# Optimization experiments

Hardware: AMD Instinct MI355X
Metric: run time of the kernel (lower is better)

## Reference

```python
import jax, jax.numpy as jnp
import numpy as np

D_EQUI = 64
D_INV = 256
D_MSG = 64
N_HEADS = 32
D_HEAD = D_INV // N_HEADS
D_FF = 256
D_EDGE_IN = 64
D_EDGE_OUT = 64
D_OUT = D_EQUI + N_HEADS + D_EDGE_OUT  # 160
IN_FEATS = 2 * D_MSG + D_EQUI + D_EDGE_IN  # 256
B, N = 4, 256


def setup_inputs() -> dict:
    key = jax.random.key(0)
    ks = jax.random.split(key, 20)
    s = 0.05
    inp = {
        "equis": jax.random.normal(ks[0], (B, N, 3, D_EQUI), jnp.float32),
        "invs": jax.random.normal(ks[1], (B, N, D_INV), jnp.float32),
        "edges": jax.random.normal(ks[2], (B, N, N, D_EDGE_IN), jnp.float32),
        "adj_matrix": jnp.ones((B, N, N), jnp.int32),
        # _PairwiseMessages params
        "qW": jax.random.normal(ks[3], (D_INV, D_MSG), jnp.float32) * s,
        "qb": jnp.zeros((D_MSG,), jnp.float32),
        "kW": jax.random.normal(ks[4], (D_INV, D_MSG), jnp.float32) * s,
        "kb": jnp.zeros((D_MSG,), jnp.float32),
        "mW1": jax.random.normal(ks[5], (IN_FEATS, D_FF), jnp.float32) * s,
        "mb1": jnp.zeros((D_FF,), jnp.float32),
        "mW2": jax.random.normal(ks[6], (D_FF, D_OUT), jnp.float32) * s,
        "mb2": jnp.zeros((D_OUT,), jnp.float32),
        # _InvAttention params
        "inv_inW": jax.random.normal(ks[7], (D_INV, D_INV), jnp.float32) * s,
        "inv_inb": jnp.zeros((D_INV,), jnp.float32),
        "inv_outW": jax.random.normal(ks[8], (D_INV, D_INV), jnp.float32) * s,
        "inv_outb": jnp.zeros((D_INV,), jnp.float32),
        # _EquiAttention params (no bias)
        "equi_inW": jax.random.normal(ks[9], (D_EQUI, D_EQUI), jnp.float32) * s,
        "equi_outW": jax.random.normal(ks[10], (D_EQUI, D_EQUI), jnp.float32) * s,
    }
    return inp


def _forward(equis, invs, edges, adj_matrix, qW, qb, kW, kb, mW1, mb1, mW2, mb2,
             inv_inW, inv_inb, inv_outW, inv_outb, equi_inW, equi_outW):
    # ---- pairwise messages ----
    # dotprods of equivariant 3-vectors per channel: [B, Nq, Nk, d_equi]
    dot = jnp.einsum("bqdc,bkdc->bqkc", equis, equis)
    qm = invs @ qW + qb  # [B,N,d_msg]
    km = invs @ kW + kb
    Nn = invs.shape[1]
    feats = jnp.concatenate([
        jnp.broadcast_to(qm[:, :, None, :], (qm.shape[0], Nn, Nn, D_MSG)),
        jnp.broadcast_to(km[:, None, :, :], (km.shape[0], Nn, Nn, D_MSG)),
        dot,
        edges,
    ], axis=-1)  # [B,N,N,in_feats]
    msgs = jax.nn.silu(feats @ mW1 + mb1) @ mW2 + mb2  # [B,N,N,d_out]

    # adjacency -> additive mask (0 where connected, -inf otherwise)
    mask = jnp.where(adj_matrix == 0, -jnp.inf, 0.0).astype(msgs.dtype)

    # ---- invariant attention (first n_heads channels) ----
    inv_msgs = msgs[..., :N_HEADS] + mask[..., None]
    attn_i = jax.nn.softmax(inv_msgs, axis=2)  # softmax over kv
    hf = (invs @ inv_inW + inv_inb).reshape(invs.shape[0], Nn, N_HEADS, D_HEAD)
    out_i = jnp.einsum("bqkh,bkhd->bqhd", attn_i, hf)
    w_i = jnp.sqrt(jnp.sum(attn_i * attn_i, axis=2))  # [B,q,H]
    out_i = out_i * w_i[..., None]
    inv_updates = out_i.reshape(invs.shape[0], Nn, D_INV) @ inv_outW + inv_outb

    # ---- equivariant attention (next d_equi channels) ----
    equi_msgs = msgs[..., N_HEADS:N_HEADS + D_EQUI] + mask[..., None]
    attn_e = jax.nn.softmax(equi_msgs, axis=2)  # [B,q,k,c]
    pe = equis @ equi_inW  # [B,N,3,d_equi]
    out_e = jnp.einsum("bqkc,bkdc->bqdc", attn_e, pe)
    w_e = jnp.sqrt(jnp.sum(attn_e * attn_e, axis=2))  # [B,q,c]
    out_e = out_e * w_e[:, :, None, :]
    equi_updates = out_e @ equi_outW  # [B,N,3,d_equi]

    # ---- edge updates (remaining channels) ----
    edge_updates = msgs[..., N_HEADS + D_EQUI:]
    return equi_updates, inv_updates, edge_updates


def reference(equis, invs, edges, adj_matrix, qW, qb, kW, kb, mW1, mb1, mW2, mb2,
              inv_inW, inv_inb, inv_outW, inv_outb, equi_inW, equi_outW):
    return _forward(equis, invs, edges, adj_matrix, qW, qb, kW, kb, mW1, mb1, mW2, mb2,
                    inv_inW, inv_inb, inv_outW, inv_outb, equi_inW, equi_outW)
```

## Files before the change

kernel.cpp:

```cpp
#include <hip/hip_runtime.h>
#include <hip/hip_bf16.h>
#include <math.h>


typedef __attribute__((ext_vector_type(8))) short short8;
typedef __attribute__((ext_vector_type(8))) __bf16 bf16x8;
typedef __attribute__((ext_vector_type(4))) float f32x4;

constexpr int EQUI_OFF = 0;
constexpr int INV_OFF  = 196608;
constexpr int EDGE_OFF = 458752;

__device__ __forceinline__ unsigned short f2bf(float x) {
    unsigned u = __builtin_bit_cast(unsigned, x);
    u = u + 0x7FFFu + ((u >> 16) & 1u);
    return (unsigned short)(u >> 16);
}
__device__ __forceinline__ float bf2f(unsigned short u) {
    return __builtin_bit_cast(float, ((unsigned)u) << 16);
}
__device__ __forceinline__ unsigned short f2bfh(float x) {
    return __builtin_bit_cast(unsigned short, (__bf16)x);
}
__device__ __forceinline__ unsigned pk2(float a, float b) {
    return (unsigned)f2bfh(a) | ((unsigned)f2bfh(b) << 16);
}
__device__ __forceinline__ short8 pk8(f32x4 a, f32x4 b) {
    bf16x8 r = { (__bf16)a.x, (__bf16)a.y, (__bf16)a.z, (__bf16)a.w,
                 (__bf16)b.x, (__bf16)b.y, (__bf16)b.z, (__bf16)b.w };
    return __builtin_bit_cast(short8, r);
}
__device__ __forceinline__ f32x4 MFMA(short8 a, short8 b, f32x4 c) {
    return __builtin_amdgcn_mfma_f32_16x16x32_bf16(
        __builtin_bit_cast(bf16x8, a), __builtin_bit_cast(bf16x8, b), c, 0, 0, 0);
}

__global__ void prep_weights(const float* __restrict__ mW1, const float* __restrict__ mW2,
                             short* __restrict__ W1T, short* __restrict__ W2T) {
    int idx = blockIdx.x * 256 + threadIdx.x;
    if (idx < 32768) {
        int n = idx >> 7, kk = idx & 127;
        W1T[idx] = (short)f2bf(mW1[(128 + kk) * 256 + n]);
    } else {
        int i2 = idx - 32768;
        int n = i2 >> 8, f = i2 & 255;
        W2T[i2] = (short)f2bf(mW2[f * 160 + n]);
    }
}

__global__ void prep_proj(const float* __restrict__ invs, const float* __restrict__ equis,
                          const float* __restrict__ qW, const float* __restrict__ qb,
                          const float* __restrict__ kW, const float* __restrict__ kb,
                          const float* __restrict__ inv_inW, const float* __restrict__ inv_inb,
                          const float* __restrict__ equi_inW,
                          float* __restrict__ qm, float* __restrict__ km,
                          float* __restrict__ hf, float* __restrict__ pe) {
    int tid = threadIdx.x;
    if (blockIdx.x < 1024) {
        int r = blockIdx.x;
        __shared__ float sInv[256];
        sInv[tid] = invs[r * 256 + tid];
        __syncthreads();
        if (tid < 64) {
            float acc = qb[tid];
            for (int f = 0; f < 256; ++f) acc += sInv[f] * qW[f * 64 + tid];
            qm[r * 64 + tid] = acc;
        } else if (tid < 128) {
            int c = tid - 64;
            float acc = kb[c];
            for (int f = 0; f < 256; ++f) acc += sInv[f] * kW[f * 64 + c];
            km[r * 64 + c] = acc;
        }
        float acch = inv_inb[tid];
        for (int f = 0; f < 256; ++f) acch += sInv[f] * inv_inW[f * 256 + tid];
        hf[r * 256 + tid] = acch;
    } else {
        int rn = blockIdx.x - 1024;
        if (tid < 192) {
            int d = tid >> 6, c = tid & 63;
            const float* erow = equis + (size_t)rn * 192 + d * 64;
            float acc = 0.f;
            for (int f = 0; f < 64; ++f) acc += erow[f] * equi_inW[f * 64 + c];
            pe[rn * 192 + d * 64 + c] = acc;
        }
    }
}

__global__ void prep_c12(const float* __restrict__ qm, const float* __restrict__ km,
                         const float* __restrict__ mW1, const float* __restrict__ mb1,
                         float* __restrict__ c1, float* __restrict__ c2) {
    int tid = threadIdx.x;
    __shared__ float s[64];
    if (blockIdx.x < 1024) {
        int r = blockIdx.x;
        if (tid < 64) s[tid] = qm[r * 64 + tid];
        __syncthreads();
        float acc = mb1[tid];
        #pragma unroll 8
        for (int k = 0; k < 64; ++k) acc = fmaf(s[k], mW1[k * 256 + tid], acc);
        c1[r * 256 + tid] = acc;
    } else {
        int r = blockIdx.x - 1024;
        if (tid < 64) s[tid] = km[r * 64 + tid];
        __syncthreads();
        float acc = 0.f;
        #pragma unroll 8
        for (int k = 0; k < 64; ++k) acc = fmaf(s[k], mW1[(64 + k) * 256 + tid], acc);
        c2[r * 256 + tid] = acc;
    }
}

__global__ void prep_T(const float* __restrict__ hf, const float* __restrict__ pe,
                       const float* __restrict__ inv_outW, const float* __restrict__ equi_outW,
                       unsigned short* __restrict__ hfT, unsigned short* __restrict__ peT,
                       unsigned short* __restrict__ WoT, unsigned short* __restrict__ EoT) {
    __shared__ float sT[64][65];
    int tid = threadIdx.x, bi = blockIdx.x;
    if (bi < 64) {
        int b = bi >> 4, t = bi & 15, tj = t >> 2, th = t & 3;
        #pragma unroll
        for (int i = 0; i < 16; ++i) { int idx = i * 256 + tid; int jl = idx >> 6, hl = idx & 63;
            sT[jl][hl] = hf[((size_t)(b * 256 + tj * 64 + jl)) * 256 + th * 64 + hl]; }
        __syncthreads();
        #pragma unroll
        for (int i = 0; i < 16; ++i) { int idx = i * 256 + tid; int hl = idx >> 6, jl = idx & 63;
            hfT[((size_t)(b * 256 + th * 64 + hl)) * 256 + tj * 64 + jl] = f2bf(sT[jl][hl]); }
    } else if (bi < 128) {
        int i2 = bi - 64; int b = i2 >> 4, t = i2 & 15, tj = t >> 2, d = t & 3;
        if (d == 3) {
            #pragma unroll
            for (int i = 0; i < 16; ++i) { int idx = i * 256 + tid; int c = idx >> 6, jl = idx & 63;
                peT[((size_t)((b * 64 + c) * 4 + 3)) * 256 + tj * 64 + jl] = 0; }
        } else {
            #pragma unroll
            for (int i = 0; i < 16; ++i) { int idx = i * 256 + tid; int jl = idx >> 6, c = idx & 63;
                sT[jl][c] = pe[((size_t)(b * 256 + tj * 64 + jl)) * 192 + d * 64 + c]; }
            __syncthreads();
            #pragma unroll
            for (int i = 0; i < 16; ++i) { int idx = i * 256 + tid; int c = idx >> 6, jl = idx & 63;
                peT[((size_t)((b * 64 + c) * 4 + d)) * 256 + tj * 64 + jl] = f2bf(sT[jl][c]); }
        }
    } else if (bi < 144) {
        int i2 = bi - 128; int tf = i2 >> 2, tn = i2 & 3;
        #pragma unroll
        for (int i = 0; i < 16; ++i) { int idx = i * 256 + tid; int fl = idx >> 6, nl = idx & 63;
            sT[fl][nl] = inv_outW[(size_t)(tf * 64 + fl) * 256 + tn * 64 + nl]; }
        __syncthreads();
        #pragma unroll
        for (int i = 0; i < 16; ++i) { int idx = i * 256 + tid; int nl = idx >> 6, fl = idx & 63;
            WoT[(size_t)(tn * 64 + nl) * 256 + tf * 64 + fl] = f2bf(sT[fl][nl]); }
    } else {
        #pragma unroll
        for (int i = 0; i < 16; ++i) { int idx = i * 256 + tid; int cl = idx >> 6, c2 = idx & 63;
            sT[cl][c2] = equi_outW[cl * 64 + c2]; }
        __syncthreads();
        #pragma unroll
        for (int i = 0; i < 16; ++i) { int idx = i * 256 + tid; int c2 = idx >> 6, cl = idx & 63;
            EoT[c2 * 64 + cl] = f2bf(sT[cl][c2]); }
    }
}

constexpr int GA_AH   = 0;
constexpr int GA_EQ   = 32768;
constexpr int GA_MASK = 33536;
constexpr int GA_BYTES = 33792;

__launch_bounds__(256, 4)
__global__ void semla_gemm(const float* __restrict__ equis, const float* __restrict__ edges,
                           const int* __restrict__ adj, const float* __restrict__ mb2,
                           const short* __restrict__ W1T, const short* __restrict__ W2T,
                           const float* __restrict__ c1, const float* __restrict__ c2,
                           float* __restrict__ out, unsigned short* __restrict__ PT) {
    extern __shared__ char smem[];
    float* sEQ   = (float*)(smem + GA_EQ);
    float* sMask = (float*)(smem + GA_MASK);

    const int tid  = threadIdx.x;
    const int lane = tid & 63;
    const int w    = tid >> 6;
    const int bid  = blockIdx.x;
    const int bq   = bid >> 2;
    const int jc   = bid & 3;
    const int b    = bq >> 8;

    const int lrow = lane & 15;
    const int kgrp = (lane >> 4) << 3;
    const int drow = (lane >> 4) << 2;

    if (tid < 192) sEQ[tid] = equis[(size_t)bq * 192 + tid];
    if (tid < 64)  sMask[tid] = adj[(size_t)bq * 256 + (jc << 6) + tid] ? 0.f : -1e30f;

    float c1v[4];
    #pragma unroll
    for (int ni = 0; ni < 4; ++ni)
        c1v[ni] = c1[bq * 256 + (w << 6) + (ni << 4) + lrow];
    const int ntiles = (w < 2) ? 3 : 2;
    const int nbase  = (w < 2) ? w * 48 : 96 + (w - 2) * 32;
    float b2v[3];
    #pragma unroll
    for (int ti = 0; ti < 3; ++ti)
        if (ti < ntiles) b2v[ti] = mb2[nbase + (ti << 4) + lrow];

    auto stA16 = [&](int row, int colbyte, short8 v) {
        int byte = ((row << 8) + colbyte) ^ ((row & 7) << 4);
        *(short8*)(smem + GA_AH + byte) = v;
    };
    auto ldA = [&](int row, int kb) -> short8 {
        int byte = ((row << 8) + (kb << 1)) ^ ((row & 7) << 4);
        return *(const short8*)(smem + GA_AH + byte);
    };
    auto stH = [&](int row, int col, unsigned short v) {
        int byte = ((row << 9) + (col << 1)) ^ ((row & 7) << 4);
        *(unsigned short*)(smem + GA_AH + byte) = v;
    };
    auto ldH = [&](int row, int kb) -> short8 {
        int byte = ((row << 9) + (kb << 1)) ^ ((row & 7) << 4);
        return *(const short8*)(smem + GA_AH + byte);
    };

    __syncthreads();

    {
        int r = tid >> 2, h = tid & 3;
        const float* erow = equis + (size_t)((b << 8) + (jc << 6) + r) * 192;
        #pragma unroll
        for (int g = 0; g < 2; ++g) {
            int cg = h + g * 4;
            f32x4 lo = (f32x4)(0.f), hi = (f32x4)(0.f);
            #pragma unroll
            for (int d = 0; d < 3; ++d) {
                f32x4 e0 = *(const f32x4*)(erow + d * 64 + cg * 8);
                f32x4 e1 = *(const f32x4*)(erow + d * 64 + cg * 8 + 4);
                f32x4 q0 = *(const f32x4*)(sEQ + d * 64 + cg * 8);
                f32x4 q1 = *(const f32x4*)(sEQ + d * 64 + cg * 8 + 4);
                lo += e0 * q0; hi += e1 * q1;
            }
            stA16(r, cg * 16, pk8(lo, hi));
        }
        const float* ebase = edges + ((size_t)bq * 256 + (jc << 6)) * 64;
        #pragma unroll
        for (int g = 0; g < 2; ++g) {
            int c8 = h + g * 4;
            f32x4 e0 = *(const f32x4*)(ebase + r * 64 + c8 * 8);
            f32x4 e1 = *(const f32x4*)(ebase + r * 64 + c8 * 8 + 4);
            stA16(r, 128 + c8 * 16, pk8(e0, e1));
        }
    }
    __syncthreads();

    f32x4 acc[4][4];
    #pragma unroll
    for (int mi = 0; mi < 4; ++mi)
        #pragma unroll
        for (int ni = 0; ni < 4; ++ni) acc[mi][ni] = (f32x4)(0.f);

    #pragma unroll
    for (int k0 = 0; k0 < 128; k0 += 32) {
        int kb = k0 + kgrp;
        short8 a0 = ldA(lrow, kb), a1 = ldA(16 + lrow, kb),
               a2 = ldA(32 + lrow, kb), a3 = ldA(48 + lrow, kb);
        short8 bf[4];
        #pragma unroll
        for (int ni = 0; ni < 4; ++ni)
            bf[ni] = *(const short8*)(W1T + ((w << 6) + (ni << 4) + lrow) * 128 + kb);
        #pragma unroll
        for (int ni = 0; ni < 4; ++ni) {
            acc[0][ni] = MFMA(a0, bf[ni], acc[0][ni]);
            acc[1][ni] = MFMA(a1, bf[ni], acc[1][ni]);
            acc[2][ni] = MFMA(a2, bf[ni], acc[2][ni]);
            acc[3][ni] = MFMA(a3, bf[ni], acc[3][ni]);
        }
    }
    __syncthreads();

    const float* c2base = c2 + ((size_t)((b << 8) + (jc << 6)) << 8);
    #pragma unroll
    for (int mi = 0; mi < 4; ++mi)
        #pragma unroll
        for (int r = 0; r < 4; ++r) {
            int row = (mi << 4) + drow + r;
            const float* c2row = c2base + (row << 8);
            #pragma unroll
            for (int ni = 0; ni < 4; ++ni) {
                int n = (w << 6) + (ni << 4) + lrow;
                float x = acc[mi][ni][r] + c1v[ni] + c2row[n];
                float hh = x * __builtin_amdgcn_rcpf(1.f + __expf(-x));
                stH(row, n, f2bfh(hh));
            }
        }
    __syncthreads();

    f32x4 acc2[4][3];
    #pragma unroll
    for (int mi = 0; mi < 4; ++mi)
        #pragma unroll
        for (int ti = 0; ti < 3; ++ti) acc2[mi][ti] = (f32x4)(0.f);

    #pragma unroll
    for (int k0 = 0; k0 < 256; k0 += 32) {
        int kb = k0 + kgrp;
        short8 a0 = ldH(lrow, kb), a1 = ldH(16 + lrow, kb),
               a2 = ldH(32 + lrow, kb), a3 = ldH(48 + lrow, kb);
        short8 bt[3];
        #pragma unroll
        for (int ti = 0; ti < 3; ++ti)
            if (ti < ntiles) bt[ti] = *(const short8*)(W2T + (nbase + (ti << 4) + lrow) * 256 + kb);
        #pragma unroll
        for (int ti = 0; ti < 3; ++ti)
            if (ti < ntiles) {
                acc2[0][ti] = MFMA(a0, bt[ti], acc2[0][ti]);
                acc2[1][ti] = MFMA(a1, bt[ti], acc2[1][ti]);
                acc2[2][ti] = MFMA(a2, bt[ti], acc2[2][ti]);
                acc2[3][ti] = MFMA(a3, bt[ti], acc2[3][ti]);
            }
    }
    __syncthreads();

    if (w < 2) {
        #pragma unroll
        for (int ti = 0; ti < 3; ++ti) {
            int n = nbase + (ti << 4) + lrow;
            float bias = b2v[ti];
            #pragma unroll
            for (int mi = 0; mi < 4; ++mi) {
                int j0 = (mi << 4) + drow;
                f32x4 mv = *(const f32x4*)(sMask + j0);
                unsigned lo = pk2(acc2[mi][ti][0] + bias + mv.x,
                                  acc2[mi][ti][1] + bias + mv.y);
                unsigned hi = pk2(acc2[mi][ti][2] + bias + mv.z,
                                  acc2[mi][ti][3] + bias + mv.w);
                *(unsigned*)(smem + n * 136 + j0 * 2)     = lo;
                *(unsigned*)(smem + n * 136 + j0 * 2 + 4) = hi;
            }
        }
    } else {
        #pragma unroll
        for (int mi = 0; mi < 4; ++mi)
            #pragma unroll
            for (int ti = 0; ti < 2; ++ti) {
                int n = nbase + (ti << 4) + lrow;
                #pragma unroll
                for (int r = 0; r < 4; ++r) {
                    int j = (jc << 6) + (mi << 4) + drow + r;
                    out[EDGE_OFF + ((size_t)bq * 256 + j) * 64 + (n - 96)] = acc2[mi][ti][r] + b2v[ti];
                }
            }
    }
    __syncthreads();

    if (tid < 192) {
        int n = tid >> 1, half = tid & 1;
        const char* src = smem + n * 136 + half * 64;
        unsigned short* dst = PT + (((size_t)bq * 96 + n) << 8) + (jc << 6) + half * 32;
        #pragma unroll
        for (int i = 0; i < 4; ++i)
            *(short8*)(dst + i * 8) = *(const short8*)(src + i * 16);
    }
}

constexpr int ES_A = 0;
constexpr int ES_W = 32768;
constexpr int ES_BYTES = 33024;

__launch_bounds__(256, 4)
__global__ void semla_einsum(const unsigned short* __restrict__ PT,
                             const unsigned short* __restrict__ hfT,
                             const unsigned short* __restrict__ peT,
                             unsigned short* __restrict__ OIb, unsigned short* __restrict__ OEb) {
    extern __shared__ char smem[];
    float* sW = (float*)(smem + ES_W);
    const int tid = threadIdx.x, lane = tid & 63, w = tid >> 6;
    const int bi = blockIdx.x;
    const int qc = bi & 3;
    const int t  = bi >> 2;
    const int b  = t / 96;
    const int c  = t - 96 * b;
    const int lrow = lane & 15, kgrp = (lane >> 4) << 3, drow = (lane >> 4) << 2;

    #pragma unroll
    for (int i = 0; i < 8; ++i) {
        int id = i * 256 + tid; int row = id >> 5, ck = id & 31;
        size_t src = (((size_t)((b << 8) + (qc << 6) + row) * 96 + c) << 8) + ck * 16;
        short8 v = *(const short8*)(PT + src);
        int byte = ((row << 9) + (ck << 4)) ^ ((row & 7) << 4);
        *(short8*)(smem + ES_A + byte) = v;
    }
    __syncthreads();

    {
        int r = tid >> 2, p = tid & 3;
        float v[64];
        #pragma unroll
        for (int i = 0; i < 8; ++i) {
            int ck = p * 8 + i;
            int byte = ((r << 9) + (ck << 4)) ^ ((r & 7) << 4);
            short8 x = *(const short8*)(smem + ES_A + byte);
            #pragma unroll
            for (int e = 0; e < 8; ++e) v[i * 8 + e] = bf2f((unsigned short)x[e]);
        }
        float m = v[0];
        #pragma unroll
        for (int i = 1; i < 64; ++i) m = fmaxf(m, v[i]);
        m = fmaxf(m, __shfl_xor(m, 1)); m = fmaxf(m, __shfl_xor(m, 2));
        float s = 0.f, q = 0.f;
        #pragma unroll
        for (int i = 0; i < 64; ++i) { float e = __expf(v[i] - m); v[i] = e; s += e; q = fmaf(e, e, q); }
        s += __shfl_xor(s, 1); s += __shfl_xor(s, 2);
        q += __shfl_xor(q, 1); q += __shfl_xor(q, 2);
        float rs = (s > 0.f) ? 1.f / s : 0.f;
        if (p == 0) sW[r] = sqrtf(q) * rs;
        #pragma unroll
        for (int i = 0; i < 8; ++i) {
            int ck = p * 8 + i;
            short8 o;
            #pragma unroll
            for (int e = 0; e < 8; ++e) o[e] = (short)f2bfh(v[i * 8 + e] * rs);
            int byte = ((r << 9) + (ck << 4)) ^ ((r & 7) << 4);
            *(short8*)(smem + ES_A + byte) = o;
        }
    }
    __syncthreads();

    const unsigned short* Bbase =
        (c < 32) ? hfT + (((size_t)((b << 8) + (c << 3) + (lrow & 7))) << 8)
                 : peT + (((size_t)((((b << 6) + (c - 32)) << 2) + (lrow & 3))) << 8);
    f32x4 acc = (f32x4)(0.f);
    #pragma unroll
    for (int k0 = 0; k0 < 256; k0 += 32) {
        int kb = k0 + kgrp;
        int byte = ((((w << 4) + lrow) << 9) + (kb << 1)) ^ ((lrow & 7) << 4);
        short8 a = *(const short8*)(smem + ES_A + byte);
        short8 bb = *(const short8*)(Bbase + kb);
        acc = MFMA(a, bb, acc);
    }
    const int nvalid = (c < 32) ? 8 : 3;
    if (lrow < nvalid) {
        #pragma unroll
        for (int r2 = 0; r2 < 4; ++r2) {
            int ql = (w << 4) + drow + r2;
            float val = acc[r2] * sW[ql];
            size_t grow = (size_t)((b << 8) + (qc << 6) + ql);
            if (c < 32) OIb[(grow << 8) + (c << 3) + lrow] = f2bfh(val);
            else        OEb[(grow * 3 + lrow) * 64 + (c - 32)] = f2bfh(val);
        }
    }
}

constexpr int PJ_BYTES = 32768;

__launch_bounds__(256, 4)
__global__ void semla_proj(const unsigned short* __restrict__ OIb,
                           const unsigned short* __restrict__ OEb,
                           const unsigned short* __restrict__ WoT,
                           const unsigned short* __restrict__ EoT,
                           const float* __restrict__ inv_outb, float* __restrict__ out) {
    extern __shared__ char smem[];
    const int tid = threadIdx.x, lane = tid & 63, w = tid >> 6;
    const int lrow = lane & 15, kgrp = (lane >> 4) << 3, drow = (lane >> 4) << 2;
    const int bi = blockIdx.x;

    if (bi < 32) {
        const int mb = bi >> 1, nb = bi & 1;
        #pragma unroll
        for (int i = 0; i < 8; ++i) {
            int id = i * 256 + tid; int row = id >> 5, ck = id & 31;
            short8 v = *(const short8*)(OIb + (((size_t)(mb * 64 + row)) << 8) + ck * 16);
            int byte = ((row << 9) + (ck << 4)) ^ ((row & 7) << 4);
            *(short8*)(smem + byte) = v;
        }
        __syncthreads();
        f32x4 acc[4][2];
        #pragma unroll
        for (int mi = 0; mi < 4; ++mi)
            #pragma unroll
            for (int ti = 0; ti < 2; ++ti) acc[mi][ti] = (f32x4)(0.f);
        #pragma unroll
        for (int k0 = 0; k0 < 256; k0 += 32) {
            int kb = k0 + kgrp;
            short8 a[4];
            #pragma unroll
            for (int mi = 0; mi < 4; ++mi) {
                int byte = ((((mi << 4) + lrow) << 9) + (kb << 1)) ^ ((lrow & 7) << 4);
                a[mi] = *(const short8*)(smem + byte);
            }
            #pragma unroll
            for (int ti = 0; ti < 2; ++ti) {
                int n = nb * 128 + w * 32 + (ti << 4) + lrow;
                short8 bb = *(const short8*)(WoT + n * 256 + kb);
                #pragma unroll
                for (int mi = 0; mi < 4; ++mi) acc[mi][ti] = MFMA(a[mi], bb, acc[mi][ti]);
            }
        }
        #pragma unroll
        for (int ti = 0; ti < 2; ++ti) {
            int n = nb * 128 + w * 32 + (ti << 4) + lrow;
            float bias = inv_outb[n];
            #pragma unroll
            for (int mi = 0; mi < 4; ++mi)
                #pragma unroll
                for (int r = 0; r < 4; ++r) {
                    int row = mb * 64 + (mi << 4) + drow + r;
                    out[INV_OFF + (size_t)row * 256 + n] = acc[mi][ti][r] + bias;
                }
        }
    } else {
        const int mb = bi - 32;
        #pragma unroll
        for (int i = 0; i < 2; ++i) {
            int id = i * 256 + tid; int row = id >> 3, ck = id & 7;
            short8 v = *(const short8*)(OEb + (((size_t)(mb * 64 + row)) << 6) + ck * 16);
            int byte = ((row << 7) + (ck << 4)) ^ ((row & 7) << 4);
            *(short8*)(smem + byte) = v;
        }
        __syncthreads();
        f32x4 acc[4];
        #pragma unroll
        for (int ni = 0; ni < 4; ++ni) acc[ni] = (f32x4)(0.f);
        #pragma unroll
        for (int k0 = 0; k0 < 64; k0 += 32) {
            int kb = k0 + kgrp;
            int byte = ((((w << 4) + lrow) << 7) + (kb << 1)) ^ ((lrow & 7) << 4);
            short8 a = *(const short8*)(smem + byte);
            #pragma unroll
            for (int ni = 0; ni < 4; ++ni) {
                short8 bb = *(const short8*)(EoT + ((ni << 4) + lrow) * 64 + kb);
                acc[ni] = MFMA(a, bb, acc[ni]);
            }
        }
        #pragma unroll
        for (int ni = 0; ni < 4; ++ni)
            #pragma unroll
            for (int r = 0; r < 4; ++r) {
                int rowg = mb * 64 + (w << 4) + drow + r;
                int bq = rowg / 3, d = rowg - 3 * bq;
                out[EQUI_OFF + (size_t)bq * 192 + d * 64 + (ni << 4) + lrow] = acc[ni][r];
            }
    }
}

extern "C" void kernel_launch(void* const* d_in, const int* in_sizes, int n_in,
                              void* d_out, int out_size, void* d_ws, size_t ws_size,
                              hipStream_t stream) {
    const float* equis    = (const float*)d_in[0];
    const float* invs     = (const float*)d_in[1];
    const float* edges    = (const float*)d_in[2];
    const int*   adj      = (const int*)d_in[3];
    const float* qW       = (const float*)d_in[4];
    const float* qb       = (const float*)d_in[5];
    const float* kW       = (const float*)d_in[6];
    const float* kb       = (const float*)d_in[7];
    const float* mW1      = (const float*)d_in[8];
    const float* mb1      = (const float*)d_in[9];
    const float* mW2      = (const float*)d_in[10];
    const float* mb2      = (const float*)d_in[11];
    const float* inv_inW  = (const float*)d_in[12];
    const float* inv_inb  = (const float*)d_in[13];
    const float* inv_outW = (const float*)d_in[14];
    const float* inv_outb = (const float*)d_in[15];
    const float* equi_inW = (const float*)d_in[16];
    const float* equi_outW= (const float*)d_in[17];

    char* ws = (char*)d_ws;
    short* W1T = (short*)(ws + 0);
    short* W2T = (short*)(ws + 65536);
    float* qm  = (float*)(ws + 147456);
    float* km  = (float*)(ws + 409600);
    float* hf  = (float*)(ws + 671744);
    float* pe  = (float*)(ws + 1720320);
    float* c1  = (float*)(ws + 2506752);
    float* c2  = (float*)(ws + 3555328);
    unsigned short* PT  = (unsigned short*)(ws + 4603904);
    unsigned short* peT = (unsigned short*)(ws + 54935552);
    unsigned short* hfT = (unsigned short*)(ws + 147456);
    unsigned short* OIb = (unsigned short*)(ws + 55459840);
    unsigned short* OEb = (unsigned short*)(ws + 55984128);
    unsigned short* WoT = (unsigned short*)(ws + 56377344);
    unsigned short* EoT = (unsigned short*)(ws + 56508416);

    prep_weights<<<288, 256, 0, stream>>>(mW1, mW2, W1T, W2T);
    prep_proj<<<2048, 256, 0, stream>>>(invs, equis, qW, qb, kW, kb,
                                        inv_inW, inv_inb, equi_inW, qm, km, hf, pe);
    prep_c12<<<2048, 256, 0, stream>>>(qm, km, mW1, mb1, c1, c2);
    prep_T<<<145, 256, 0, stream>>>(hf, pe, inv_outW, equi_outW, hfT, peT, WoT, EoT);
    semla_gemm<<<4096, 256, GA_BYTES, stream>>>(equis, edges, adj, mb2, W1T, W2T,
                                                c1, c2, (float*)d_out, PT);
    semla_einsum<<<1536, 256, ES_BYTES, stream>>>(PT, hfT, peT, OIb, OEb);
    semla_proj<<<80, 256, PJ_BYTES, stream>>>(OIb, OEb, WoT, EoT, inv_outb, (float*)d_out);
}
```

Before: 167.2 us.

## Merge prep kernels and loop semla_gemm over key chunks with edge prefetch

```diff
diff --git a/kernel.cpp b/kernel.cpp
--- a/kernel.cpp
+++ b/kernel.cpp
@@ -35,29 +35,18 @@
         __builtin_bit_cast(bf16x8, a), __builtin_bit_cast(bf16x8, b), c, 0, 0, 0);
 }
 
-__global__ void prep_weights(const float* __restrict__ mW1, const float* __restrict__ mW2,
-                             short* __restrict__ W1T, short* __restrict__ W2T) {
-    int idx = blockIdx.x * 256 + threadIdx.x;
-    if (idx < 32768) {
-        int n = idx >> 7, kk = idx & 127;
-        W1T[idx] = (short)f2bf(mW1[(128 + kk) * 256 + n]);
-    } else {
-        int i2 = idx - 32768;
-        int n = i2 >> 8, f = i2 & 255;
-        W2T[i2] = (short)f2bf(mW2[f * 160 + n]);
-    }
-}
-
-__global__ void prep_proj(const float* __restrict__ invs, const float* __restrict__ equis,
-                          const float* __restrict__ qW, const float* __restrict__ qb,
-                          const float* __restrict__ kW, const float* __restrict__ kb,
-                          const float* __restrict__ inv_inW, const float* __restrict__ inv_inb,
-                          const float* __restrict__ equi_inW,
-                          float* __restrict__ qm, float* __restrict__ km,
-                          float* __restrict__ hf, float* __restrict__ pe) {
-    int tid = threadIdx.x;
-    if (blockIdx.x < 1024) {
-        int r = blockIdx.x;
+__global__ void prep1(const float* __restrict__ invs, const float* __restrict__ equis,
+                      const float* __restrict__ qW, const float* __restrict__ qb,
+                      const float* __restrict__ kW, const float* __restrict__ kb,
+                      const float* __restrict__ inv_inW, const float* __restrict__ inv_inb,
+                      const float* __restrict__ equi_inW,
+                      const float* __restrict__ mW1, const float* __restrict__ mW2,
+                      float* __restrict__ qm, float* __restrict__ km,
+                      float* __restrict__ hf, float* __restrict__ pe,
+                      short* __restrict__ W1T, short* __restrict__ W2T) {
+    int tid = threadIdx.x, bi = blockIdx.x;
+    if (bi < 1024) {
+        int r = bi;
         __shared__ float sInv[256];
         sInv[tid] = invs[r * 256 + tid];
         __syncthreads();
@@ -74,8 +63,8 @@
         float acch = inv_inb[tid];
         for (int f = 0; f < 256; ++f) acch += sInv[f] * inv_inW[f * 256 + tid];
         hf[r * 256 + tid] = acch;
-    } else {
-        int rn = blockIdx.x - 1024;
+    } else if (bi < 2048) {
+        int rn = bi - 1024;
         if (tid < 192) {
             int d = tid >> 6, c = tid & 63;
             const float* erow = equis + (size_t)rn * 192 + d * 64;
@@ -83,87 +72,95 @@
             for (int f = 0; f < 64; ++f) acc += erow[f] * equi_inW[f * 64 + c];
             pe[rn * 192 + d * 64 + c] = acc;
         }
-    }
-}
-
-__global__ void prep_c12(const float* __restrict__ qm, const float* __restrict__ km,
-                         const float* __restrict__ mW1, const float* __restrict__ mb1,
-                         float* __restrict__ c1, float* __restrict__ c2) {
-    int tid = threadIdx.x;
-    __shared__ float s[64];
-    if (blockIdx.x < 1024) {
-        int r = blockIdx.x;
-        if (tid < 64) s[tid] = qm[r * 64 + tid];
+    } else {
+        int idx = (bi - 2048) * 256 + tid;
+        if (idx < 32768) {
+            int n = idx >> 7, kk = idx & 127;
+            W1T[idx] = (short)f2bf(mW1[(128 + kk) * 256 + n]);
+        } else {
+            int i2 = idx - 32768;
+            int n = i2 >> 8, f = i2 & 255;
+            W2T[i2] = (short)f2bf(mW2[f * 160 + n]);
+        }
+    }
+}
+
+__global__ void prep2(const float* __restrict__ qm, const float* __restrict__ km,
+                      const float* __restrict__ mW1, const float* __restrict__ mb1,
+                      const float* __restrict__ hf, const float* __restrict__ pe,
+                      const float* __restrict__ inv_outW, const float* __restrict__ equi_outW,
+                      float* __restrict__ c1, float* __restrict__ c2,
+                      unsigned short* __restrict__ hfT, unsigned short* __restrict__ peT,
+                      unsigned short* __restrict__ WoT, unsigned short* __restrict__ EoT) {
+    __shared__ float sT[64][65];
+    int tid = threadIdx.x, bi = blockIdx.x;
+    if (bi < 1024) {
+        int r = bi;
+        if (tid < 64) sT[0][tid] = qm[r * 64 + tid];
         __syncthreads();
         float acc = mb1[tid];
         #pragma unroll 8
-        for (int k = 0; k < 64; ++k) acc = fmaf(s[k], mW1[k * 256 + tid], acc);
+        for (int k = 0; k < 64; ++k) acc = fmaf(sT[0][k], mW1[k * 256 + tid], acc);
         c1[r * 256 + tid] = acc;
-    } else {
-        int r = blockIdx.x - 1024;
-        if (tid < 64) s[tid] = km[r * 64 + tid];
+    } else if (bi < 2048) {
+        int r = bi - 1024;
+        if (tid < 64) sT[0][tid] = km[r * 64 + tid];
         __syncthreads();
         float acc = 0.f;
         #pragma unroll 8
-        for (int k = 0; k < 64; ++k) acc = fmaf(s[k], mW1[(64 + k) * 256 + tid], acc);
+        for (int k = 0; k < 64; ++k) acc = fmaf(sT[0][k], mW1[(64 + k) * 256 + tid], acc);
         c2[r * 256 + tid] = acc;
-    }
-}
-
-__global__ void prep_T(const float* __restrict__ hf, const float* __restrict__ pe,
-                       const float* __restrict__ inv_outW, const float* __restrict__ equi_outW,
-                       unsigned short* __restrict__ hfT, unsigned short* __restrict__ peT,
-                       unsigned short* __restrict__ WoT, unsigned short* __restrict__ EoT) {
-    __shared__ float sT[64][65];
-    int tid = threadIdx.x, bi = blockIdx.x;
-    if (bi < 64) {
-        int b = bi >> 4, t = bi & 15, tj = t >> 2, th = t & 3;
-        #pragma unroll
-        for (int i = 0; i < 16; ++i) { int idx = i * 256 + tid; int jl = idx >> 6, hl = idx & 63;
-            sT[jl][hl] = hf[((size_t)(b * 256 + tj * 64 + jl)) * 256 + th * 64 + hl]; }
-        __syncthreads();
-        #pragma unroll
-        for (int i = 0; i < 16; ++i) { int idx = i * 256 + tid; int hl = idx >> 6, jl = idx & 63;
-            hfT[((size_t)(b * 256 + th * 64 + hl)) * 256 + tj * 64 + jl] = f2bf(sT[jl][hl]); }
-    } else if (bi < 128) {
-        int i2 = bi - 64; int b = i2 >> 4, t = i2 & 15, tj = t >> 2, d = t & 3;
-        if (d == 3) {
-            #pragma unroll
-            for (int i = 0; i < 16; ++i) { int idx = i * 256 + tid; int c = idx >> 6, jl = idx & 63;
-                peT[((size_t)((b * 64 + c) * 4 + 3)) * 256 + tj * 64 + jl] = 0; }
+    } else {
+        int bt = bi - 2048;
+        if (bt < 64) {
+            int b = bt >> 4, t = bt & 15, tj = t >> 2, th = t & 3;
+            #pragma unroll
+            for (int i = 0; i < 16; ++i) { int idx = i * 256 + tid; int jl = idx >> 6, hl = idx & 63;
+                sT[jl][hl] = hf[((size_t)(b * 256 + tj * 64 + jl)) * 256 + th * 64 + hl]; }
+            __syncthreads();
+            #pragma unroll
+            for (int i = 0; i < 16; ++i) { int idx = i * 256 + tid; int hl = idx >> 6, jl = idx & 63;
+                hfT[((size_t)(b * 256 + th * 64 + hl)) * 256 + tj * 64 + jl] = f2bf(sT[jl][hl]); }
+        } else if (bt < 128) {
+            int i2 = bt - 64; int b = i2 >> 4, t = i2 & 15, tj = t >> 2, d = t & 3;
+            if (d == 3) {
+                #pragma unroll
+                for (int i = 0; i < 16; ++i) { int idx = i * 256 + tid; int c = idx >> 6, jl = idx & 63;
+                    peT[((size_t)((b * 64 + c) * 4 + 3)) * 256 + tj * 64 + jl] = 0; }
+            } else {
+                #pragma unroll
+                for (int i = 0; i < 16; ++i) { int idx = i * 256 + tid; int jl = idx >> 6, c = idx & 63;
+                    sT[jl][c] = pe[((size_t)(b * 256 + tj * 64 + jl)) * 192 + d * 64 + c]; }
+                __syncthreads();
+                #pragma unroll
+                for (int i = 0; i < 16; ++i) { int idx = i * 256 + tid; int c = idx >> 6, jl = idx & 63;
+                    peT[((size_t)((b * 64 + c) * 4 + d)) * 256 + tj * 64 + jl] = f2bf(sT[jl][c]); }
+            }
+        } else if (bt < 144) {
+            int i2 = bt - 128; int tf = i2 >> 2, tn = i2 & 3;
+            #pragma unroll
+            for (int i = 0; i < 16; ++i) { int idx = i * 256 + tid; int fl = idx >> 6, nl = idx & 63;
+                sT[fl][nl] = inv_outW[(size_t)(tf * 64 + fl) * 256 + tn * 64 + nl]; }
+            __syncthreads();
+            #pragma unroll
+            for (int i = 0; i < 16; ++i) { int idx = i * 256 + tid; int nl = idx >> 6, fl = idx & 63;
+                WoT[(size_t)(tn * 64 + nl) * 256 + tf * 64 + fl] = f2bf(sT[fl][nl]); }
         } else {
             #pragma unroll
-            for (int i = 0; i < 16; ++i) { int idx = i * 256 + tid; int jl = idx >> 6, c = idx & 63;
-                sT[jl][c] = pe[((size_t)(b * 256 + tj * 64 + jl)) * 192 + d * 64 + c]; }
+            for (int i = 0; i < 16; ++i) { int idx = i * 256 + tid; int cl = idx >> 6, c2i = idx & 63;
+                sT[cl][c2i] = equi_outW[cl * 64 + c2i]; }
             __syncthreads();
             #pragma unroll
-            for (int i = 0; i < 16; ++i) { int idx = i * 256 + tid; int c = idx >> 6, jl = idx & 63;
-                peT[((size_t)((b * 64 + c) * 4 + d)) * 256 + tj * 64 + jl] = f2bf(sT[jl][c]); }
-        }
-    } else if (bi < 144) {
-        int i2 = bi - 128; int tf = i2 >> 2, tn = i2 & 3;
-        #pragma unroll
-        for (int i = 0; i < 16; ++i) { int idx = i * 256 + tid; int fl = idx >> 6, nl = idx & 63;
-            sT[fl][nl] = inv_outW[(size_t)(tf * 64 + fl) * 256 + tn * 64 + nl]; }
-        __syncthreads();
-        #pragma unroll
-        for (int i = 0; i < 16; ++i) { int idx = i * 256 + tid; int nl = idx >> 6, fl = idx & 63;
-            WoT[(size_t)(tn * 64 + nl) * 256 + tf * 64 + fl] = f2bf(sT[fl][nl]); }
-    } else {
-        #pragma unroll
-        for (int i = 0; i < 16; ++i) { int idx = i * 256 + tid; int cl = idx >> 6, c2 = idx & 63;
-            sT[cl][c2] = equi_outW[cl * 64 + c2]; }
-        __syncthreads();
-        #pragma unroll
-        for (int i = 0; i < 16; ++i) { int idx = i * 256 + tid; int c2 = idx >> 6, cl = idx & 63;
-            EoT[c2 * 64 + cl] = f2bf(sT[cl][c2]); }
+            for (int i = 0; i < 16; ++i) { int idx = i * 256 + tid; int c2i = idx >> 6, cl = idx & 63;
+                EoT[c2i * 64 + cl] = f2bf(sT[cl][c2i]); }
+        }
     }
 }
 
 constexpr int GA_AH   = 0;
 constexpr int GA_EQ   = 32768;
 constexpr int GA_MASK = 33536;
-constexpr int GA_BYTES = 33792;
+constexpr int GA_BYTES = 34560;
 
 __launch_bounds__(256, 4)
 __global__ void semla_gemm(const float* __restrict__ equis, const float* __restrict__ edges,
@@ -178,17 +175,26 @@
     const int tid  = threadIdx.x;
     const int lane = tid & 63;
     const int w    = tid >> 6;
-    const int bid  = blockIdx.x;
-    const int bq   = bid >> 2;
-    const int jc   = bid & 3;
+    const int bq   = (blockIdx.x & 7) * 128 + (blockIdx.x >> 3);
     const int b    = bq >> 8;
 
     const int lrow = lane & 15;
     const int kgrp = (lane >> 4) << 3;
     const int drow = (lane >> 4) << 2;
+    const int r    = tid >> 2, h = tid & 3;
+
+    const float* ebq = edges + (size_t)bq * 16384;
+    f32x4 ed0, ed1, ed2, ed3;
+    {
+        const float* eb = ebq + r * 64;
+        ed0 = *(const f32x4*)(eb + h * 8);
+        ed1 = *(const f32x4*)(eb + h * 8 + 4);
+        ed2 = *(const f32x4*)(eb + (h + 4) * 8);
+        ed3 = *(const f32x4*)(eb + (h + 4) * 8 + 4);
+    }
 
     if (tid < 192) sEQ[tid] = equis[(size_t)bq * 192 + tid];
-    if (tid < 64)  sMask[tid] = adj[(size_t)bq * 256 + (jc << 6) + tid] ? 0.f : -1e30f;
+    sMask[tid] = adj[(size_t)bq * 256 + tid] ? 0.f : -1e30f;
 
     float c1v[4];
     #pragma unroll
@@ -218,143 +224,148 @@
         return *(const short8*)(smem + GA_AH + byte);
     };
 
-    __syncthreads();
-
-    {
-        int r = tid >> 2, h = tid & 3;
-        const float* erow = equis + (size_t)((b << 8) + (jc << 6) + r) * 192;
-        #pragma unroll
-        for (int g = 0; g < 2; ++g) {
-            int cg = h + g * 4;
-            f32x4 lo = (f32x4)(0.f), hi = (f32x4)(0.f);
-            #pragma unroll
-            for (int d = 0; d < 3; ++d) {
-                f32x4 e0 = *(const f32x4*)(erow + d * 64 + cg * 8);
-                f32x4 e1 = *(const f32x4*)(erow + d * 64 + cg * 8 + 4);
-                f32x4 q0 = *(const f32x4*)(sEQ + d * 64 + cg * 8);
-                f32x4 q1 = *(const f32x4*)(sEQ + d * 64 + cg * 8 + 4);
-                lo += e0 * q0; hi += e1 * q1;
-            }
-            stA16(r, cg * 16, pk8(lo, hi));
-        }
-        const float* ebase = edges + ((size_t)bq * 256 + (jc << 6)) * 64;
-        #pragma unroll
-        for (int g = 0; g < 2; ++g) {
-            int c8 = h + g * 4;
-            f32x4 e0 = *(const f32x4*)(ebase + r * 64 + c8 * 8);
-            f32x4 e1 = *(const f32x4*)(ebase + r * 64 + c8 * 8 + 4);
-            stA16(r, 128 + c8 * 16, pk8(e0, e1));
-        }
-    }
-    __syncthreads();
-
-    f32x4 acc[4][4];
-    #pragma unroll
-    for (int mi = 0; mi < 4; ++mi)
-        #pragma unroll
-        for (int ni = 0; ni < 4; ++ni) acc[mi][ni] = (f32x4)(0.f);
-
-    #pragma unroll
-    for (int k0 = 0; k0 < 128; k0 += 32) {
-        int kb = k0 + kgrp;
-        short8 a0 = ldA(lrow, kb), a1 = ldA(16 + lrow, kb),
-               a2 = ldA(32 + lrow, kb), a3 = ldA(48 + lrow, kb);
-        short8 bf[4];
-        #pragma unroll
-        for (int ni = 0; ni < 4; ++ni)
-            bf[ni] = *(const short8*)(W1T + ((w << 6) + (ni << 4) + lrow) * 128 + kb);
-        #pragma unroll
-        for (int ni = 0; ni < 4; ++ni) {
-            acc[0][ni] = MFMA(a0, bf[ni], acc[0][ni]);
-            acc[1][ni] = MFMA(a1, bf[ni], acc[1][ni]);
-            acc[2][ni] = MFMA(a2, bf[ni], acc[2][ni]);
-            acc[3][ni] = MFMA(a3, bf[ni], acc[3][ni]);
-        }
-    }
-    __syncthreads();
-
-    const float* c2base = c2 + ((size_t)((b << 8) + (jc << 6)) << 8);
-    #pragma unroll
-    for (int mi = 0; mi < 4; ++mi)
-        #pragma unroll
-        for (int r = 0; r < 4; ++r) {
-            int row = (mi << 4) + drow + r;
-            const float* c2row = c2base + (row << 8);
+    #pragma unroll 1
+    for (int jc = 0; jc < 4; ++jc) {
+        __syncthreads();
+
+        {
+            const float* erow = equis + (size_t)((b << 8) + (jc << 6) + r) * 192;
+            #pragma unroll
+            for (int g = 0; g < 2; ++g) {
+                int cg = h + g * 4;
+                f32x4 lo = (f32x4)(0.f), hi = (f32x4)(0.f);
+                #pragma unroll
+                for (int d = 0; d < 3; ++d) {
+                    f32x4 e0 = *(const f32x4*)(erow + d * 64 + cg * 8);
+                    f32x4 e1 = *(const f32x4*)(erow + d * 64 + cg * 8 + 4);
+                    f32x4 q0 = *(const f32x4*)(sEQ + d * 64 + cg * 8);
+                    f32x4 q1 = *(const f32x4*)(sEQ + d * 64 + cg * 8 + 4);
+                    lo += e0 * q0; hi += e1 * q1;
+                }
+                stA16(r, cg * 16, pk8(lo, hi));
+            }
+            stA16(r, 128 + h * 16,       pk8(ed0, ed1));
+            stA16(r, 128 + (h + 4) * 16, pk8(ed2, ed3));
+        }
+        __syncthreads();
+
+        f32x4 acc[4][4];
+        #pragma unroll
+        for (int mi = 0; mi < 4; ++mi)
+            #pragma unroll
+            for (int ni = 0; ni < 4; ++ni) acc[mi][ni] = (f32x4)(0.f);
+
+        #pragma unroll
+        for (int k0 = 0; k0 < 128; k0 += 32) {
+            int kb = k0 + kgrp;
+            short8 a0 = ldA(lrow, kb), a1 = ldA(16 + lrow, kb),
+                   a2 = ldA(32 + lrow, kb), a3 = ldA(48 + lrow, kb);
+            short8 bf[4];
+            #pragma unroll
+            for (int ni = 0; ni < 4; ++ni)
+                bf[ni] = *(const short8*)(W1T + ((w << 6) + (ni << 4) + lrow) * 128 + kb);
             #pragma unroll
             for (int ni = 0; ni < 4; ++ni) {
-                int n = (w << 6) + (ni << 4) + lrow;
-                float x = acc[mi][ni][r] + c1v[ni] + c2row[n];
-                float hh = x * __builtin_amdgcn_rcpf(1.f + __expf(-x));
-                stH(row, n, f2bfh(hh));
-            }
-        }
-    __syncthreads();
-
-    f32x4 acc2[4][3];
-    #pragma unroll
-    for (int mi = 0; mi < 4; ++mi)
-        #pragma unroll
-        for (int ti = 0; ti < 3; ++ti) acc2[mi][ti] = (f32x4)(0.f);
-
-    #pragma unroll
-    for (int k0 = 0; k0 < 256; k0 += 32) {
-        int kb = k0 + kgrp;
-        short8 a0 = ldH(lrow, kb), a1 = ldH(16 + lrow, kb),
-               a2 = ldH(32 + lrow, kb), a3 = ldH(48 + lrow, kb);
-        short8 bt[3];
-        #pragma unroll
-        for (int ti = 0; ti < 3; ++ti)
-            if (ti < ntiles) bt[ti] = *(const short8*)(W2T + (nbase + (ti << 4) + lrow) * 256 + kb);
-        #pragma unroll
-        for (int ti = 0; ti < 3; ++ti)
-            if (ti < ntiles) {
-                acc2[0][ti] = MFMA(a0, bt[ti], acc2[0][ti]);
-                acc2[1][ti] = MFMA(a1, bt[ti], acc2[1][ti]);
-                acc2[2][ti] = MFMA(a2, bt[ti], acc2[2][ti]);
-                acc2[3][ti] = MFMA(a3, bt[ti], acc2[3][ti]);
-            }
-    }
-    __syncthreads();
-
-    if (w < 2) {
-        #pragma unroll
-        for (int ti = 0; ti < 3; ++ti) {
-            int n = nbase + (ti << 4) + lrow;
-            float bias = b2v[ti];
-            #pragma unroll
-            for (int mi = 0; mi < 4; ++mi) {
-                int j0 = (mi << 4) + drow;
-                f32x4 mv = *(const f32x4*)(sMask + j0);
-                unsigned lo = pk2(acc2[mi][ti][0] + bias + mv.x,
-                                  acc2[mi][ti][1] + bias + mv.y);
-                unsigned hi = pk2(acc2[mi][ti][2] + bias + mv.z,
-                                  acc2[mi][ti][3] + bias + mv.w);
-                *(unsigned*)(smem + n * 136 + j0 * 2)     = lo;
-                *(unsigned*)(smem + n * 136 + j0 * 2 + 4) = hi;
-            }
-        }
-    } else {
+                acc[0][ni] = MFMA(a0, bf[ni], acc[0][ni]);
+                acc[1][ni] = MFMA(a1, bf[ni], acc[1][ni]);
+                acc[2][ni] = MFMA(a2, bf[ni], acc[2][ni]);
+                acc[3][ni] = MFMA(a3, bf[ni], acc[3][ni]);
+            }
+        }
+        __syncthreads();
+
+        const float* c2base = c2 + ((size_t)((b << 8) + (jc << 6)) << 8);
         #pragma unroll
         for (int mi = 0; mi < 4; ++mi)
             #pragma unroll
-            for (int ti = 0; ti < 2; ++ti) {
+            for (int rr = 0; rr < 4; ++rr) {
+                int row = (mi << 4) + drow + rr;
+                const float* c2row = c2base + (row << 8);
+                #pragma unroll
+                for (int ni = 0; ni < 4; ++ni) {
+                    int n = (w << 6) + (ni << 4) + lrow;
+                    float x = acc[mi][ni][rr] + c1v[ni] + c2row[n];
+                    float hh = x * __builtin_amdgcn_rcpf(1.f + __expf(-x));
+                    stH(row, n, f2bfh(hh));
+                }
+            }
+
+        {
+            int jn = (jc + 1) & 3;
+            const float* eb = ebq + ((jn << 6) + r) * 64;
+            ed0 = *(const f32x4*)(eb + h * 8);
+            ed1 = *(const f32x4*)(eb + h * 8 + 4);
+            ed2 = *(const f32x4*)(eb + (h + 4) * 8);
+            ed3 = *(const f32x4*)(eb + (h + 4) * 8 + 4);
+        }
+        __syncthreads();
+
+        f32x4 acc2[4][3];
+        #pragma unroll
+        for (int mi = 0; mi < 4; ++mi)
+            #pragma unroll
+            for (int ti = 0; ti < 3; ++ti) acc2[mi][ti] = (f32x4)(0.f);
+
+        #pragma unroll
+        for (int k0 = 0; k0 < 256; k0 += 32) {
+            int kb = k0 + kgrp;
+            short8 a0 = ldH(lrow, kb), a1 = ldH(16 + lrow, kb),
+                   a2 = ldH(32 + lrow, kb), a3 = ldH(48 + lrow, kb);
+            short8 bt[3];
+            #pragma unroll
+            for (int ti = 0; ti < 3; ++ti)
+                if (ti < ntiles) bt[ti] = *(const short8*)(W2T + (nbase + (ti << 4) + lrow) * 256 + kb);
+            #pragma unroll
+            for (int ti = 0; ti < 3; ++ti)
+                if (ti < ntiles) {
+                    acc2[0][ti] = MFMA(a0, bt[ti], acc2[0][ti]);
+                    acc2[1][ti] = MFMA(a1, bt[ti], acc2[1][ti]);
+                    acc2[2][ti] = MFMA(a2, bt[ti], acc2[2][ti]);
+                    acc2[3][ti] = MFMA(a3, bt[ti], acc2[3][ti]);
+                }
+        }
+        __syncthreads();
+
+        if (w < 2) {
+            #pragma unroll
+            for (int ti = 0; ti < 3; ++ti) {
                 int n = nbase + (ti << 4) + lrow;
-                #pragma unroll
-                for (int r = 0; r < 4; ++r) {
-                    int j = (jc << 6) + (mi << 4) + drow + r;
-                    out[EDGE_OFF + ((size_t)bq * 256 + j) * 64 + (n - 96)] = acc2[mi][ti][r] + b2v[ti];
+                float bias = b2v[ti];
+                #pragma unroll
+                for (int mi = 0; mi < 4; ++mi) {
+                    int j0 = (mi << 4) + drow;
+                    f32x4 mv = *(const f32x4*)(sMask + (jc << 6) + j0);
+                    unsigned lo = pk2(acc2[mi][ti][0] + bias + mv.x,
+                                      acc2[mi][ti][1] + bias + mv.y);
+                    unsigned hi = pk2(acc2[mi][ti][2] + bias + mv.z,
+                                      acc2[mi][ti][3] + bias + mv.w);
+                    *(unsigned*)(smem + n * 136 + j0 * 2)     = lo;
+                    *(unsigned*)(smem + n * 136 + j0 * 2 + 4) = hi;
                 }
             }
-    }
-    __syncthreads();
-
-    if (tid < 192) {
-        int n = tid >> 1, half = tid & 1;
-        const char* src = smem + n * 136 + half * 64;
-        unsigned short* dst = PT + (((size_t)bq * 96 + n) << 8) + (jc << 6) + half * 32;
-        #pragma unroll
-        for (int i = 0; i < 4; ++i)
-            *(short8*)(dst + i * 8) = *(const short8*)(src + i * 16);
+        } else {
+            #pragma unroll
+            for (int mi = 0; mi < 4; ++mi)
+                #pragma unroll
+                for (int ti = 0; ti < 2; ++ti) {
+                    int n = nbase + (ti << 4) + lrow;
+                    #pragma unroll
+                    for (int rr = 0; rr < 4; ++rr) {
+                        int j = (jc << 6) + (mi << 4) + drow + rr;
+                        out[EDGE_OFF + ((size_t)bq * 256 + j) * 64 + (n - 96)] = acc2[mi][ti][rr] + b2v[ti];
+                    }
+                }
+        }
+        __syncthreads();
+
+        if (tid < 192) {
+            int n = tid >> 1, half = tid & 1;
+            const char* src = smem + n * 136 + half * 64;
+            unsigned short* dst = PT + (((size_t)bq * 96 + n) << 8) + (jc << 6) + half * 32;
+            #pragma unroll
+            for (int i = 0; i < 4; ++i)
+                *(short8*)(dst + i * 8) = *(const short8*)(src + i * 16);
+        }
     }
 }
 
@@ -498,9 +509,9 @@
             #pragma unroll
             for (int mi = 0; mi < 4; ++mi)
                 #pragma unroll
-                for (int r = 0; r < 4; ++r) {
-                    int row = mb * 64 + (mi << 4) + drow + r;
-                    out[INV_OFF + (size_t)row * 256 + n] = acc[mi][ti][r] + bias;
+                for (int rr = 0; rr < 4; ++rr) {
+                    int row = mb * 64 + (mi << 4) + drow + rr;
+                    out[INV_OFF + (size_t)row * 256 + n] = acc[mi][ti][rr] + bias;
                 }
         }
     } else {
@@ -530,10 +541,10 @@
         #pragma unroll
         for (int ni = 0; ni < 4; ++ni)
             #pragma unroll
-            for (int r = 0; r < 4; ++r) {
-                int rowg = mb * 64 + (w << 4) + drow + r;
+            for (int rr = 0; rr < 4; ++rr) {
+                int rowg = mb * 64 + (w << 4) + drow + rr;
                 int bq = rowg / 3, d = rowg - 3 * bq;
-                out[EQUI_OFF + (size_t)bq * 192 + d * 64 + (ni << 4) + lrow] = acc[ni][r];
+                out[EQUI_OFF + (size_t)bq * 192 + d * 64 + (ni << 4) + lrow] = acc[ni][rr];
             }
     }
 }
@@ -571,18 +582,18 @@
     float* c2  = (float*)(ws + 3555328);
     unsigned short* PT  = (unsigned short*)(ws + 4603904);
     unsigned short* peT = (unsigned short*)(ws + 54935552);
-    unsigned short* hfT = (unsigned short*)(ws + 147456);
-    unsigned short* OIb = (unsigned short*)(ws + 55459840);
-    unsigned short* OEb = (unsigned short*)(ws + 55984128);
-    unsigned short* WoT = (unsigned short*)(ws + 56377344);
-    unsigned short* EoT = (unsigned short*)(ws + 56508416);
-
-    prep_weights<<<288, 256, 0, stream>>>(mW1, mW2, W1T, W2T);
-    prep_proj<<<2048, 256, 0, stream>>>(invs, equis, qW, qb, kW, kb,
-                                        inv_inW, inv_inb, equi_inW, qm, km, hf, pe);
-    prep_c12<<<2048, 256, 0, stream>>>(qm, km, mW1, mb1, c1, c2);
-    prep_T<<<145, 256, 0, stream>>>(hf, pe, inv_outW, equi_outW, hfT, peT, WoT, EoT);
-    semla_gemm<<<4096, 256, GA_BYTES, stream>>>(equis, edges, adj, mb2, W1T, W2T,
+    unsigned short* hfT = (unsigned short*)(ws + 55459840);
+    unsigned short* OIb = (unsigned short*)(ws + 55984128);
+    unsigned short* OEb = (unsigned short*)(ws + 56508416);
+    unsigned short* WoT = (unsigned short*)(ws + 56901632);
+    unsigned short* EoT = (unsigned short*)(ws + 57032704);
+
+    prep1<<<2336, 256, 0, stream>>>(invs, equis, qW, qb, kW, kb,
+                                    inv_inW, inv_inb, equi_inW, mW1, mW2,
+                                    qm, km, hf, pe, W1T, W2T);
+    prep2<<<2193, 256, 0, stream>>>(qm, km, mW1, mb1, hf, pe, inv_outW, equi_outW,
+                                    c1, c2, hfT, peT, WoT, EoT);
+    semla_gemm<<<1024, 256, GA_BYTES, stream>>>(equis, edges, adj, mb2, W1T, W2T,
                                                 c1, c2, (float*)d_out, PT);
     semla_einsum<<<1536, 256, ES_BYTES, stream>>>(PT, hfT, peT, OIb, OEb);
     semla_proj<<<80, 256, PJ_BYTES, stream>>>(OIb, OEb, WoT, EoT, inv_outb, (float*)d_out);
```

Measured after the change: 597.0 us. 257% more time.
